# Optimization experiments

Measured on AMD Instinct MI355X. Metric: run time of the kernel, lower is better.

The kernel has to match this reference:

```python
import jax, jax.numpy as jnp
import numpy as np

L, B, C_IN, C_OUT, C_COND = 4096, 16, 512, 512, 512
K, RATIO, TEMPERATURE = 4, 4, 30.0
HID = C_COND // RATIO


def setup_inputs() -> dict:
    key = jax.random.key(0)
    ks = jax.random.split(key, 8)
    s_in = 1.0 / np.sqrt(C_IN)
    s_c = 1.0 / np.sqrt(C_COND)
    s_h = 1.0 / np.sqrt(HID)
    return {
        "x": jax.random.normal(ks[0], (L, B, C_IN), jnp.float32),
        "cond": jax.random.normal(ks[1], (B, C_COND), jnp.float32),
        "fc1_w": jax.random.normal(ks[2], (HID, C_COND), jnp.float32) * s_c,
        "fc1_b": jnp.zeros((HID,), jnp.float32),
        "fc2_w": jax.random.normal(ks[3], (K, HID), jnp.float32) * s_h,
        "fc2_b": jnp.zeros((K,), jnp.float32),
        "weight": jax.random.normal(ks[4], (K, C_OUT, C_IN), jnp.float32) * s_in,
        "bias": jax.random.normal(ks[5], (K, C_OUT), jnp.float32) * s_in,
    }


def reference(x, cond, fc1_w, fc1_b, fc2_w, fc2_b, weight, bias):
    # attention over K kernel banks, conditioned on style vector
    h = jax.nn.relu(cond @ fc1_w.T + fc1_b)          # (B, HID)
    logits = h @ fc2_w.T + fc2_b                     # (B, K)
    att = jax.nn.softmax(logits / TEMPERATURE, axis=-1)
    # per-sample aggregated 1x1-conv weight/bias (the grouped conv, groups=B)
    w_agg = jnp.einsum("bk,koi->boi", att, weight)   # (B, C_OUT, C_IN)
    b_agg = att @ bias                               # (B, C_OUT)
    # per-sample matmul over tokens: (L,B,C_in) x (B,C_out,C_in) -> (L,B,C_out)
    out = jnp.einsum("lbi,boi->lbo", x, w_agg) + b_agg[None, :, :]
    return out
```

## Files before the change

kernel.cpp:

```cpp
#include <hip/hip_runtime.h>
#include <hip/hip_bf16.h>

typedef __bf16 bfx8 __attribute__((ext_vector_type(8)));
typedef float f32x4 __attribute__((ext_vector_type(4)));
typedef unsigned short u16x8 __attribute__((ext_vector_type(8)));
typedef unsigned short u16x4 __attribute__((ext_vector_type(4)));

__device__ __forceinline__ unsigned short f2bf(float f) {
    unsigned int u = __builtin_bit_cast(unsigned int, f);
    u += 0x7fffu + ((u >> 16) & 1u);
    return (unsigned short)(u >> 16);
}

__device__ __forceinline__ int swz_idx(int row, int chunk) {
    const int p = row >> 1;
    const int q = (((row & 1) << 2) | chunk) ^ (p & 7);
    return p * 64 + q * 8;
}

__global__ __launch_bounds__(1024) void att_kernel(
    const float* __restrict__ cond, const float* __restrict__ fc1w,
    const float* __restrict__ fc1b, const float* __restrict__ fc2w,
    const float* __restrict__ fc2b, const float* __restrict__ bias,
    float* __restrict__ att_out, float* __restrict__ bagg_out)
{
    __shared__ float h[128];
    __shared__ float att_s[4];
    const int b    = blockIdx.x;
    const int tid  = threadIdx.x;
    const int lane = tid & 63;
    const int wv   = tid >> 6;

    for (int j = wv; j < 128; j += 16) {
        const float* c = cond + b * 512 + lane * 8;
        const float* w = fc1w + j * 512 + lane * 8;
        const float4 c0 = *(const float4*)c, c1 = *(const float4*)(c + 4);
        const float4 w0 = *(const float4*)w, w1 = *(const float4*)(w + 4);
        float s = c0.x * w0.x + c0.y * w0.y + c0.z * w0.z + c0.w * w0.w
                + c1.x * w1.x + c1.y * w1.y + c1.z * w1.z + c1.w * w1.w;
        #pragma unroll
        for (int off = 32; off; off >>= 1) s += __shfl_down(s, off);
        if (lane == 0) h[j] = fmaxf(s + fc1b[j], 0.0f);
    }
    __syncthreads();

    if (wv < 4) {
        const int k = wv;
        float s = h[lane] * fc2w[k * 128 + lane] + h[lane + 64] * fc2w[k * 128 + lane + 64];
        #pragma unroll
        for (int off = 32; off; off >>= 1) s += __shfl_down(s, off);
        if (lane == 0) att_s[k] = (s + fc2b[k]) * (1.0f / 30.0f);
    }
    __syncthreads();

    if (tid == 0) {
        float l0 = att_s[0], l1 = att_s[1], l2 = att_s[2], l3 = att_s[3];
        float m = fmaxf(fmaxf(l0, l1), fmaxf(l2, l3));
        float e0 = expf(l0 - m), e1 = expf(l1 - m), e2 = expf(l2 - m), e3 = expf(l3 - m);
        float inv = 1.0f / (e0 + e1 + e2 + e3);
        att_s[0] = e0 * inv; att_s[1] = e1 * inv; att_s[2] = e2 * inv; att_s[3] = e3 * inv;
        att_out[b * 4 + 0] = att_s[0]; att_out[b * 4 + 1] = att_s[1];
        att_out[b * 4 + 2] = att_s[2]; att_out[b * 4 + 3] = att_s[3];
    }
    __syncthreads();

    if (tid < 512) {
        bagg_out[b * 512 + tid] = att_s[0] * bias[tid] + att_s[1] * bias[512 + tid]
                                + att_s[2] * bias[1024 + tid] + att_s[3] * bias[1536 + tid];
    }
}

__global__ __launch_bounds__(256) void wagg_kernel(
    const float* __restrict__ weight, const float* __restrict__ att,
    unsigned short* __restrict__ wagg)
{
    __shared__ float a_s[64];
    if (threadIdx.x < 64) a_s[threadIdx.x] = att[threadIdx.x];
    __syncthreads();
    const int p = (blockIdx.x * 256 + threadIdx.x) * 4;
    const float4 w0 = *(const float4*)(weight + p);
    const float4 w1 = *(const float4*)(weight + 262144 + p);
    const float4 w2 = *(const float4*)(weight + 524288 + p);
    const float4 w3 = *(const float4*)(weight + 786432 + p);
    #pragma unroll
    for (int b = 0; b < 16; ++b) {
        const float a0 = a_s[4 * b], a1 = a_s[4 * b + 1], a2 = a_s[4 * b + 2], a3 = a_s[4 * b + 3];
        u16x4 r;
        r[0] = f2bf(a0 * w0.x + a1 * w1.x + a2 * w2.x + a3 * w3.x);
        r[1] = f2bf(a0 * w0.y + a1 * w1.y + a2 * w2.y + a3 * w3.y);
        r[2] = f2bf(a0 * w0.z + a1 * w1.z + a2 * w2.z + a3 * w3.z);
        r[3] = f2bf(a0 * w0.w + a1 * w1.w + a2 * w2.w + a3 * w3.w);
        *(u16x4*)(wagg + (size_t)b * 262144 + p) = r;
    }
}

__global__ __launch_bounds__(512, 2) void gemm_kernel(
    const float* __restrict__ x, const unsigned short* __restrict__ wagg,
    const float* __restrict__ bagg, float* __restrict__ out)
{
    __shared__ unsigned short As[2][256 * 32];
    __shared__ unsigned short Bs[2][256 * 32];
    __shared__ float bsh[256];

    const int tid = threadIdx.x;
    const int bid = (blockIdx.x & 7) * 64 + (blockIdx.x >> 3);
    const int b  = bid >> 5;
    const int lt = (bid >> 1) & 15;
    const int nt = bid & 1;
    const int l0 = lt * 256;
    const int n0 = nt * 256;

    const int lane = tid & 63;
    const int wid  = tid >> 6;
    const int wm   = wid >> 2;
    const int wn   = wid & 3;
    const int fr   = lane & 15;
    const int fq   = lane >> 4;

    const unsigned short* wb = wagg + (size_t)b * (512 * 512) + (size_t)n0 * 512;

    if (tid < 256) bsh[tid] = bagg[b * 512 + n0 + tid];

    f32x4 acc[8][4];
    #pragma unroll
    for (int i = 0; i < 8; ++i)
        #pragma unroll
        for (int j = 0; j < 4; ++j) acc[i][j] = f32x4{0.f, 0.f, 0.f, 0.f};

    const int arow = tid >> 1;
    const int acb  = (tid & 1) * 2;
    const int aswz0 = swz_idx(arow, acb);
    const int aswz1 = swz_idx(arow, acb + 1);
    const float* xsrc = x + ((size_t)(l0 + arow) * 16 + b) * 512 + (tid & 1) * 16;

    int bofs[2];
    #pragma unroll
    for (int it = 0; it < 2; ++it) {
        const int s = tid + it * 512;
        const int p = s >> 3, q = s & 7;
        const int v = q ^ (p & 7);
        const int row = (p << 1) | (v >> 2);
        const int cch = v & 3;
        bofs[it] = row * 512 + cch * 8;
    }

    int aidx[8], bidx[4];
    #pragma unroll
    for (int mf = 0; mf < 8; ++mf) aidx[mf] = swz_idx(wm * 128 + mf * 16 + fr, fq);
    #pragma unroll
    for (int nf = 0; nf < 4; ++nf) bidx[nf] = swz_idx(wn * 64 + nf * 16 + fr, fq);

    float4 xv0, xv1, xv2, xv3;
    {
        const float4 v0 = *(const float4*)(xsrc);
        const float4 v1 = *(const float4*)(xsrc + 4);
        const float4 v2 = *(const float4*)(xsrc + 8);
        const float4 v3 = *(const float4*)(xsrc + 12);
        u16x8 pk;
        pk[0] = f2bf(v0.x); pk[1] = f2bf(v0.y); pk[2] = f2bf(v0.z); pk[3] = f2bf(v0.w);
        pk[4] = f2bf(v1.x); pk[5] = f2bf(v1.y); pk[6] = f2bf(v1.z); pk[7] = f2bf(v1.w);
        *(u16x8*)&As[0][aswz0] = pk;
        pk[0] = f2bf(v2.x); pk[1] = f2bf(v2.y); pk[2] = f2bf(v2.z); pk[3] = f2bf(v2.w);
        pk[4] = f2bf(v3.x); pk[5] = f2bf(v3.y); pk[6] = f2bf(v3.z); pk[7] = f2bf(v3.w);
        *(u16x8*)&As[0][aswz1] = pk;
        #pragma unroll
        for (int it = 0; it < 2; ++it) {
            char* dst = (char*)&Bs[0][0] + (tid + it * 512) * 16;
            __builtin_amdgcn_global_load_lds(
                (const __attribute__((address_space(1))) void*)(wb + bofs[it]),
                (__attribute__((address_space(3))) void*)dst, 16, 0, 0);
        }
        xv0 = *(const float4*)(xsrc + 32);
        xv1 = *(const float4*)(xsrc + 36);
        xv2 = *(const float4*)(xsrc + 40);
        xv3 = *(const float4*)(xsrc + 44);
    }
    asm volatile("s_waitcnt vmcnt(4) lgkmcnt(0)" ::: "memory");
    __builtin_amdgcn_s_barrier();

    int cur = 0;
    for (int kt = 0; kt < 16; ++kt) {
        const int nxt = cur ^ 1;
        float4 xn0, xn1, xn2, xn3;
        if (kt < 15) {
            const int k0n = (kt + 1) * 32;
            #pragma unroll
            for (int it = 0; it < 2; ++it) {
                char* dst = (char*)&Bs[nxt][0] + (tid + it * 512) * 16;
                __builtin_amdgcn_global_load_lds(
                    (const __attribute__((address_space(1))) void*)(wb + bofs[it] + k0n),
                    (__attribute__((address_space(3))) void*)dst, 16, 0, 0);
            }
            __builtin_amdgcn_sched_barrier(0);
            const int kp = (kt + 2 <= 15) ? (kt + 2) * 32 : 15 * 32;
            xn0 = *(const float4*)(xsrc + kp);
            xn1 = *(const float4*)(xsrc + kp + 4);
            xn2 = *(const float4*)(xsrc + kp + 8);
            xn3 = *(const float4*)(xsrc + kp + 12);
            __builtin_amdgcn_sched_barrier(0);
        }
        bfx8 bfr[4];
        #pragma unroll
        for (int nf = 0; nf < 4; ++nf)
            bfr[nf] = *reinterpret_cast<const bfx8*>(&Bs[cur][bidx[nf]]);
        #pragma unroll
        for (int mf = 0; mf < 8; ++mf) {
            const bfx8 af = *reinterpret_cast<const bfx8*>(&As[cur][aidx[mf]]);
            #pragma unroll
            for (int nf = 0; nf < 4; ++nf)
                acc[mf][nf] = __builtin_amdgcn_mfma_f32_16x16x32_bf16(af, bfr[nf], acc[mf][nf], 0, 0, 0);
        }
        if (kt < 15) {
            u16x8 pk;
            pk[0] = f2bf(xv0.x); pk[1] = f2bf(xv0.y); pk[2] = f2bf(xv0.z); pk[3] = f2bf(xv0.w);
            pk[4] = f2bf(xv1.x); pk[5] = f2bf(xv1.y); pk[6] = f2bf(xv1.z); pk[7] = f2bf(xv1.w);
            *(u16x8*)&As[nxt][aswz0] = pk;
            pk[0] = f2bf(xv2.x); pk[1] = f2bf(xv2.y); pk[2] = f2bf(xv2.z); pk[3] = f2bf(xv2.w);
            pk[4] = f2bf(xv3.x); pk[5] = f2bf(xv3.y); pk[6] = f2bf(xv3.z); pk[7] = f2bf(xv3.w);
            *(u16x8*)&As[nxt][aswz1] = pk;
            asm volatile("s_waitcnt vmcnt(4) lgkmcnt(0)" ::: "memory");
            __builtin_amdgcn_s_barrier();
            cur = nxt;
            xv0 = xn0; xv1 = xn1; xv2 = xn2; xv3 = xn3;
        }
    }

    #pragma unroll
    for (int mf = 0; mf < 8; ++mf) {
        #pragma unroll
        for (int nf = 0; nf < 4; ++nf) {
            const int on = wn * 64 + nf * 16 + fr;
            const float bb = bsh[on];
            const int lrow = l0 + wm * 128 + mf * 16 + fq * 4;
            float* op = out + ((size_t)lrow * 16 + b) * 512 + n0 + on;
            const f32x4 a = acc[mf][nf];
            op[0]        = a[0] + bb;
            op[8192]     = a[1] + bb;
            op[2 * 8192] = a[2] + bb;
            op[3 * 8192] = a[3] + bb;
        }
    }
}

extern "C" void kernel_launch(void* const* d_in, const int* in_sizes, int n_in,
                              void* d_out, int out_size, void* d_ws, size_t ws_size,
                              hipStream_t stream) {
    const float* x      = (const float*)d_in[0];
    const float* cond   = (const float*)d_in[1];
    const float* fc1w   = (const float*)d_in[2];
    const float* fc1b   = (const float*)d_in[3];
    const float* fc2w   = (const float*)d_in[4];
    const float* fc2b   = (const float*)d_in[5];
    const float* weight = (const float*)d_in[6];
    const float* bias   = (const float*)d_in[7];
    float* out = (float*)d_out;

    char* ws = (char*)d_ws;
    float* att_ws  = (float*)ws;
    float* bagg_ws = (float*)(ws + 1024);
    unsigned short* wagg_ws = (unsigned short*)(ws + 65536);

    att_kernel<<<16, 1024, 0, stream>>>(cond, fc1w, fc1b, fc2w, fc2b, bias, att_ws, bagg_ws);
    wagg_kernel<<<256, 256, 0, stream>>>(weight, att_ws, wagg_ws);
    gemm_kernel<<<512, 512, 0, stream>>>(x, wagg_ws, bagg_ws, out);
}
```

Baseline: 103.7 us.

## Double K-tile to 64 and split GEMM main loop into four barrier-synchronized phases

```diff
diff --git a/kernel.cpp b/kernel.cpp
--- a/kernel.cpp
+++ b/kernel.cpp
@@ -10,12 +10,6 @@
     unsigned int u = __builtin_bit_cast(unsigned int, f);
     u += 0x7fffu + ((u >> 16) & 1u);
     return (unsigned short)(u >> 16);
-}
-
-__device__ __forceinline__ int swz_idx(int row, int chunk) {
-    const int p = row >> 1;
-    const int q = (((row & 1) << 2) | chunk) ^ (p & 7);
-    return p * 64 + q * 8;
 }
 
 __global__ __launch_bounds__(1024) void att_kernel(
@@ -98,8 +92,8 @@
     const float* __restrict__ x, const unsigned short* __restrict__ wagg,
     const float* __restrict__ bagg, float* __restrict__ out)
 {
-    __shared__ unsigned short As[2][256 * 32];
-    __shared__ unsigned short Bs[2][256 * 32];
+    __shared__ unsigned short As[2][256 * 64];
+    __shared__ unsigned short Bs[2][256 * 64];
     __shared__ float bsh[256];
 
     const int tid = threadIdx.x;
@@ -128,102 +122,129 @@
         for (int j = 0; j < 4; ++j) acc[i][j] = f32x4{0.f, 0.f, 0.f, 0.f};
 
     const int arow = tid >> 1;
-    const int acb  = (tid & 1) * 2;
-    const int aswz0 = swz_idx(arow, acb);
-    const int aswz1 = swz_idx(arow, acb + 1);
-    const float* xsrc = x + ((size_t)(l0 + arow) * 16 + b) * 512 + (tid & 1) * 16;
-
-    int bofs[2];
-    #pragma unroll
-    for (int it = 0; it < 2; ++it) {
-        const int s = tid + it * 512;
-        const int p = s >> 3, q = s & 7;
-        const int v = q ^ (p & 7);
-        const int row = (p << 1) | (v >> 2);
-        const int cch = v & 3;
-        bofs[it] = row * 512 + cch * 8;
-    }
-
-    int aidx[8], bidx[4];
-    #pragma unroll
-    for (int mf = 0; mf < 8; ++mf) aidx[mf] = swz_idx(wm * 128 + mf * 16 + fr, fq);
-    #pragma unroll
-    for (int nf = 0; nf < 4; ++nf) bidx[nf] = swz_idx(wn * 64 + nf * 16 + fr, fq);
-
-    float4 xv0, xv1, xv2, xv3;
+    const int ach  = (tid & 1) * 4;
+    const float* xsrc = x + ((size_t)(l0 + arow) * 16 + b) * 512 + (tid & 1) * 32;
+    int awr[4];
+    #pragma unroll
+    for (int j = 0; j < 4; ++j)
+        awr[j] = arow * 64 + (((ach + j) ^ (arow & 7)) << 3);
+
+    int bofs[4], bdst[4];
+    #pragma unroll
+    for (int it = 0; it < 4; ++it) {
+        const int s  = it * 512 + tid;
+        const int rw = s >> 3, cd = s & 7;
+        const int cs = cd ^ (rw & 7);
+        bofs[it] = rw * 512 + cs * 8;
+        bdst[it] = s * 16;
+    }
+
+    int abase[8], bbase[4], koff[2];
+    #pragma unroll
+    for (int mf = 0; mf < 8; ++mf) abase[mf] = (wm * 128 + mf * 16 + fr) * 64;
+    #pragma unroll
+    for (int nf = 0; nf < 4; ++nf) bbase[nf] = (wn * 64 + nf * 16 + fr) * 64;
+    #pragma unroll
+    for (int ks = 0; ks < 2; ++ks) koff[ks] = (((ks * 4 + fq) ^ (fr & 7)) << 3);
+
     {
-        const float4 v0 = *(const float4*)(xsrc);
-        const float4 v1 = *(const float4*)(xsrc + 4);
-        const float4 v2 = *(const float4*)(xsrc + 8);
-        const float4 v3 = *(const float4*)(xsrc + 12);
-        u16x8 pk;
-        pk[0] = f2bf(v0.x); pk[1] = f2bf(v0.y); pk[2] = f2bf(v0.z); pk[3] = f2bf(v0.w);
-        pk[4] = f2bf(v1.x); pk[5] = f2bf(v1.y); pk[6] = f2bf(v1.z); pk[7] = f2bf(v1.w);
-        *(u16x8*)&As[0][aswz0] = pk;
-        pk[0] = f2bf(v2.x); pk[1] = f2bf(v2.y); pk[2] = f2bf(v2.z); pk[3] = f2bf(v2.w);
-        pk[4] = f2bf(v3.x); pk[5] = f2bf(v3.y); pk[6] = f2bf(v3.z); pk[7] = f2bf(v3.w);
-        *(u16x8*)&As[0][aswz1] = pk;
-        #pragma unroll
-        for (int it = 0; it < 2; ++it) {
-            char* dst = (char*)&Bs[0][0] + (tid + it * 512) * 16;
+        #pragma unroll
+        for (int it = 0; it < 4; ++it) {
+            char* dst = (char*)&Bs[0][0] + bdst[it];
             __builtin_amdgcn_global_load_lds(
                 (const __attribute__((address_space(1))) void*)(wb + bofs[it]),
                 (__attribute__((address_space(3))) void*)dst, 16, 0, 0);
         }
-        xv0 = *(const float4*)(xsrc + 32);
-        xv1 = *(const float4*)(xsrc + 36);
-        xv2 = *(const float4*)(xsrc + 40);
-        xv3 = *(const float4*)(xsrc + 44);
-    }
-    asm volatile("s_waitcnt vmcnt(4) lgkmcnt(0)" ::: "memory");
-    __builtin_amdgcn_s_barrier();
+        float4 v[8];
+        #pragma unroll
+        for (int j = 0; j < 8; ++j) v[j] = *(const float4*)(xsrc + j * 4);
+        #pragma unroll
+        for (int j = 0; j < 4; ++j) {
+            u16x8 pk;
+            pk[0] = f2bf(v[2*j].x);   pk[1] = f2bf(v[2*j].y);
+            pk[2] = f2bf(v[2*j].z);   pk[3] = f2bf(v[2*j].w);
+            pk[4] = f2bf(v[2*j+1].x); pk[5] = f2bf(v[2*j+1].y);
+            pk[6] = f2bf(v[2*j+1].z); pk[7] = f2bf(v[2*j+1].w);
+            *(u16x8*)&As[0][awr[j]] = pk;
+        }
+        asm volatile("s_waitcnt vmcnt(0) lgkmcnt(0)" ::: "memory");
+        __builtin_amdgcn_s_barrier();
+    }
+
+#define PHASE(MQ, NQ, TAIL_ASM)                                                   \
+    do {                                                                          \
+        const unsigned short* Ac = &As[cur][0];                                   \
+        const unsigned short* Bc = &Bs[cur][0];                                   \
+        bfx8 afr[4][2], bfr[2][2];                                                \
+        _Pragma("unroll")                                                         \
+        for (int i = 0; i < 4; ++i)                                               \
+            _Pragma("unroll")                                                     \
+            for (int ks = 0; ks < 2; ++ks)                                        \
+                afr[i][ks] = *(const bfx8*)&Ac[abase[(MQ)*4 + i] + koff[ks]];     \
+        _Pragma("unroll")                                                         \
+        for (int j = 0; j < 2; ++j)                                               \
+            _Pragma("unroll")                                                     \
+            for (int ks = 0; ks < 2; ++ks)                                        \
+                bfr[j][ks] = *(const bfx8*)&Bc[bbase[(NQ)*2 + j] + koff[ks]];     \
+        __builtin_amdgcn_s_barrier();                                             \
+        asm volatile("s_waitcnt lgkmcnt(0)" ::: "memory");                        \
+        __builtin_amdgcn_sched_barrier(0);                                        \
+        __builtin_amdgcn_s_setprio(1);                                            \
+        _Pragma("unroll")                                                         \
+        for (int ks = 0; ks < 2; ++ks)                                            \
+            _Pragma("unroll")                                                     \
+            for (int i = 0; i < 4; ++i)                                           \
+                _Pragma("unroll")                                                 \
+                for (int j = 0; j < 2; ++j)                                       \
+                    acc[(MQ)*4 + i][(NQ)*2 + j] =                                 \
+                        __builtin_amdgcn_mfma_f32_16x16x32_bf16(                  \
+                            afr[i][ks], bfr[j][ks],                               \
+                            acc[(MQ)*4 + i][(NQ)*2 + j], 0, 0, 0);                \
+        __builtin_amdgcn_s_setprio(0);                                            \
+        TAIL_ASM;                                                                 \
+        __builtin_amdgcn_s_barrier();                                             \
+    } while (0)
 
     int cur = 0;
-    for (int kt = 0; kt < 16; ++kt) {
+    for (int t = 0; t < 8; ++t) {
         const int nxt = cur ^ 1;
-        float4 xn0, xn1, xn2, xn3;
-        if (kt < 15) {
-            const int k0n = (kt + 1) * 32;
+        float4 xv[8];
+        if (t < 7) {
+            const int ko = (t + 1) * 64;
             #pragma unroll
-            for (int it = 0; it < 2; ++it) {
-                char* dst = (char*)&Bs[nxt][0] + (tid + it * 512) * 16;
+            for (int j = 0; j < 8; ++j) xv[j] = *(const float4*)(xsrc + ko + j * 4);
+            __builtin_amdgcn_sched_barrier(0);
+        }
+        PHASE(0, 0, );
+        if (t < 7) {
+            const int ko = (t + 1) * 64;
+            #pragma unroll
+            for (int it = 0; it < 4; ++it) {
+                char* dst = (char*)&Bs[nxt][0] + bdst[it];
                 __builtin_amdgcn_global_load_lds(
-                    (const __attribute__((address_space(1))) void*)(wb + bofs[it] + k0n),
+                    (const __attribute__((address_space(1))) void*)(wb + bofs[it] + ko),
                     (__attribute__((address_space(3))) void*)dst, 16, 0, 0);
             }
             __builtin_amdgcn_sched_barrier(0);
-            const int kp = (kt + 2 <= 15) ? (kt + 2) * 32 : 15 * 32;
-            xn0 = *(const float4*)(xsrc + kp);
-            xn1 = *(const float4*)(xsrc + kp + 4);
-            xn2 = *(const float4*)(xsrc + kp + 8);
-            xn3 = *(const float4*)(xsrc + kp + 12);
+        }
+        PHASE(0, 1, );
+        PHASE(1, 0, );
+        if (t < 7) {
+            #pragma unroll
+            for (int j = 0; j < 4; ++j) {
+                u16x8 pk;
+                pk[0] = f2bf(xv[2*j].x);   pk[1] = f2bf(xv[2*j].y);
+                pk[2] = f2bf(xv[2*j].z);   pk[3] = f2bf(xv[2*j].w);
+                pk[4] = f2bf(xv[2*j+1].x); pk[5] = f2bf(xv[2*j+1].y);
+                pk[6] = f2bf(xv[2*j+1].z); pk[7] = f2bf(xv[2*j+1].w);
+                *(u16x8*)&As[nxt][awr[j]] = pk;
+            }
             __builtin_amdgcn_sched_barrier(0);
         }
-        bfx8 bfr[4];
-        #pragma unroll
-        for (int nf = 0; nf < 4; ++nf)
-            bfr[nf] = *reinterpret_cast<const bfx8*>(&Bs[cur][bidx[nf]]);
-        #pragma unroll
-        for (int mf = 0; mf < 8; ++mf) {
-            const bfx8 af = *reinterpret_cast<const bfx8*>(&As[cur][aidx[mf]]);
-            #pragma unroll
-            for (int nf = 0; nf < 4; ++nf)
-                acc[mf][nf] = __builtin_amdgcn_mfma_f32_16x16x32_bf16(af, bfr[nf], acc[mf][nf], 0, 0, 0);
-        }
-        if (kt < 15) {
-            u16x8 pk;
-            pk[0] = f2bf(xv0.x); pk[1] = f2bf(xv0.y); pk[2] = f2bf(xv0.z); pk[3] = f2bf(xv0.w);
-            pk[4] = f2bf(xv1.x); pk[5] = f2bf(xv1.y); pk[6] = f2bf(xv1.z); pk[7] = f2bf(xv1.w);
-            *(u16x8*)&As[nxt][aswz0] = pk;
-            pk[0] = f2bf(xv2.x); pk[1] = f2bf(xv2.y); pk[2] = f2bf(xv2.z); pk[3] = f2bf(xv2.w);
-            pk[4] = f2bf(xv3.x); pk[5] = f2bf(xv3.y); pk[6] = f2bf(xv3.z); pk[7] = f2bf(xv3.w);
-            *(u16x8*)&As[nxt][aswz1] = pk;
-            asm volatile("s_waitcnt vmcnt(4) lgkmcnt(0)" ::: "memory");
-            __builtin_amdgcn_s_barrier();
-            cur = nxt;
-            xv0 = xn0; xv1 = xn1; xv2 = xn2; xv3 = xn3;
-        }
-    }
+        PHASE(1, 1, asm volatile("s_waitcnt vmcnt(0)" ::: "memory"));
+        cur = nxt;
+    }
+#undef PHASE
 
     #pragma unroll
     for (int mf = 0; mf < 8; ++mf) {
```

After: 114.0 us. 9.9% more time.
